# Kernel tuning notes

Hardware: AMD Instinct MI355X
Metric: run time of the kernel (lower is better)

Reference implementation:

```python
import jax, jax.numpy as jnp
import numpy as np

B, S, H = 2, 2048, 1024
NH = 16
HD = H // NH  # 64


def setup_inputs() -> dict:
    key = jax.random.key(0)
    ks = jax.random.split(key, 12)
    s = 1.0 / np.sqrt(H)
    return {
        "x_q": jax.random.normal(ks[0], (B, S, H), jnp.float32),
        "x_k": jax.random.normal(ks[1], (B, S, H), jnp.float32),
        "x_v": jax.random.normal(ks[2], (B, S, H), jnp.float32),
        "attention_mask": jax.random.randint(ks[3], (B, S), 0, 2, jnp.int32),
        "Wq": jax.random.normal(ks[4], (H, H), jnp.float32) * s,
        "bq": jnp.zeros((H,), jnp.float32),
        "Wk": jax.random.normal(ks[5], (H, H), jnp.float32) * s,
        "bk": jnp.zeros((H,), jnp.float32),
        "Wv": jax.random.normal(ks[6], (H, H), jnp.float32) * s,
        "bv": jnp.zeros((H,), jnp.float32),
        "Wo": jax.random.normal(ks[7], (H, H), jnp.float32) * s,
        "bo": jnp.zeros((H,), jnp.float32),
    }


def reference(x_q, x_k, x_v, attention_mask, Wq, bq, Wk, bk, Wv, bv, Wo, bo):
    b, s, h = x_q.shape
    # projections
    q = x_q @ Wq + bq
    k = x_k @ Wk + bk
    v = x_v @ Wv + bv
    # [B, NH, S, HD]
    q = q.reshape(b, s, NH, HD).transpose(0, 2, 1, 3)
    k = k.reshape(b, s, NH, HD).transpose(0, 2, 1, 3)
    v = v.reshape(b, s, NH, HD).transpose(0, 2, 1, 3)
    scores = jnp.einsum("bhqd,bhkd->bhqk", q, k) / jnp.sqrt(jnp.float32(HD))
    # key-padding mask: 1 -> keep (0 bias), else -inf; broadcast [B,1,1,S]
    bias = jnp.where(attention_mask == 1, 0.0, -jnp.inf).astype(scores.dtype)
    scores = scores + bias[:, None, None, :]
    attn = jax.nn.softmax(scores, axis=-1)
    # dropout prob = 0.0 (eval / deterministic): identity
    out = jnp.einsum("bhqk,bhkd->bhqd", attn, v)
    out = out.transpose(0, 2, 1, 3).reshape(b, s, h)
    return out @ Wo + bo
```

## Files before the change

### kernel.cpp

```cpp
#include <hip/hip_runtime.h>

#define DEVI static __device__ __forceinline__

typedef unsigned short u16;
typedef unsigned int u32;
typedef __attribute__((ext_vector_type(8))) __bf16 bf16x8;
typedef __attribute__((ext_vector_type(8))) short short8;
typedef __attribute__((ext_vector_type(4))) float f32x4;
typedef __attribute__((ext_vector_type(16))) float f32x16;
typedef __attribute__((ext_vector_type(4))) u32 u32x4;

DEVI u16 f2bf(float f) {
  union { float f; u32 u; } v; v.f = f;
  u32 r = v.u + 0x7fffu + ((v.u >> 16) & 1u);
  return (u16)(r >> 16);
}

DEVI u16 bfc(float f) {
  union { __bf16 b; u16 u; } v; v.b = (__bf16)f; return v.u;
}

DEVI u32 pk2bf(float lo, float hi) {
  union { struct { __bf16 l, h; } s; u32 u; } c;
  c.s.l = (__bf16)lo; c.s.h = (__bf16)hi;
  return c.u;
}

DEVI void gload16(const void* g, void* l) {
  __builtin_amdgcn_global_load_lds(
      (const __attribute__((address_space(1))) void*)g,
      (__attribute__((address_space(3))) void*)l,
      16, 0, 0);
}

__global__ void k_prep(const float* __restrict__ W0, const float* __restrict__ W1,
                       const float* __restrict__ W2, const float* __restrict__ W3,
                       u16* __restrict__ Wtb,
                       const int* __restrict__ msk, float* __restrict__ bias,
                       const float* __restrict__ xq, const float* __restrict__ xk,
                       const float* __restrict__ xv, u16* __restrict__ xbf) {
  const int z = blockIdx.z;
  const int tid = threadIdx.y * 32 + threadIdx.x;
  if (z == 4) {
    if (blockIdx.x < 16 && blockIdx.y == 0) {
      const int i = blockIdx.x * 256 + tid;
      bias[i] = (msk[i] == 1) ? 0.f : -1e30f;
    }
    return;
  }
  if (z >= 5) {
    const int xi = z - 5;
    const float* in = (xi == 0) ? xq : ((xi == 1) ? xk : xv);
    u16* out = xbf + (size_t)xi * 4194304;
    const int lin = (blockIdx.y * 32 + blockIdx.x) * 256 + tid;
#pragma unroll
    for (int j = 0; j < 4; ++j) {
      const int idx = j * 262144 + lin;
      const float4 v = reinterpret_cast<const float4*>(in)[idx];
      ushort4 s;
      s.x = f2bf(v.x); s.y = f2bf(v.y); s.z = f2bf(v.z); s.w = f2bf(v.w);
      reinterpret_cast<ushort4*>(out)[idx] = s;
    }
    return;
  }
  const float* W = (z == 0) ? W0 : ((z == 1) ? W1 : ((z == 2) ? W2 : W3));
  u16* Wt = Wtb + (size_t)z * 1024 * 1024;
  __shared__ float tl[32][33];
  const int n0 = blockIdx.x * 32, k0 = blockIdx.y * 32;
  const int tx = threadIdx.x, ty = threadIdx.y;
#pragma unroll
  for (int r = ty; r < 32; r += 8)
    tl[r][tx] = W[(size_t)(k0 + r) * 1024 + n0 + tx];
  __syncthreads();
#pragma unroll
  for (int r = ty; r < 32; r += 8)
    Wt[(size_t)(n0 + r) * 1024 + k0 + tx] = f2bf(tl[tx][r]);
}

DEVI void store1(u16* C, size_t i, float v) { C[i] = f2bf(v); }
DEVI void store1(float* C, size_t i, float v) { C[i] = v; }

template <typename OutT, int BN>
__global__ __launch_bounds__(256, 2) void k_gemm_bt(
    const u16* __restrict__ Abase, long aZ,
    const u16* __restrict__ Btbase, long bZ,
    const float* __restrict__ bias0, const float* __restrict__ bias1,
    const float* __restrict__ bias2,
    float s0, float s1, float s2,
    OutT* __restrict__ Cbase, long cZ, u16* __restrict__ Vt,
    int M, int N, int K) {
  const int z = blockIdx.z;
  const u16* A  = Abase + (size_t)z * aZ;
  const u16* Bt = Btbase + (size_t)z * bZ;
  OutT* C = Cbase + (size_t)z * cZ;
  const float* bias = (z == 0) ? bias0 : ((z == 1) ? bias1 : bias2);
  const float scl = (z == 0) ? s0 : ((z == 1) ? s1 : s2);

  constexpr int NF = BN / 32;
  __shared__ u16 lsA[128 * 32];
  __shared__ u16 lsB[BN * 32];

  const int t = threadIdx.x;
  const int w = t >> 6, ln = t & 63;
  const int l15 = ln & 15, lhi = ln >> 4;
  const int wr = w >> 1, wc = w & 1;
  const int m0 = blockIdx.x * 128, n0 = blockIdx.y * BN;

  f32x4 acc[4][NF] = {};

  for (int kt = 0; kt < K; kt += 32) {
#pragma unroll
    for (int i = 0; i < 2; ++i) {
      const int li = i * 256 + t;
      const int row = li >> 2, cb = (li & 3) << 3;
      gload16(A + (size_t)(m0 + row) * K + kt + cb,
              (char*)lsA + (i * 256 + w * 64) * 16);
    }
#pragma unroll
    for (int i = 0; i < BN / 64; ++i) {
      const int li = i * 256 + t;
      const int row = li >> 2, cb = (li & 3) << 3;
      gload16(Bt + (size_t)(n0 + row) * K + kt + cb,
              (char*)lsB + (i * 256 + w * 64) * 16);
    }
    __syncthreads();

    bf16x8 af[4], bf_[NF];
#pragma unroll
    for (int m = 0; m < 4; ++m)
      af[m] = *reinterpret_cast<const bf16x8*>(
          &lsA[(wr * 64 + m * 16 + l15) * 32 + lhi * 8]);
#pragma unroll
    for (int n = 0; n < NF; ++n)
      bf_[n] = *reinterpret_cast<const bf16x8*>(
          &lsB[(wc * (BN / 2) + n * 16 + l15) * 32 + lhi * 8]);
#pragma unroll
    for (int m = 0; m < 4; ++m)
#pragma unroll
      for (int n = 0; n < NF; ++n)
        acc[m][n] = __builtin_amdgcn_mfma_f32_16x16x32_bf16(af[m], bf_[n], acc[m][n], 0, 0, 0);
    __syncthreads();
  }

  if (Vt != nullptr && z == 2) {
#pragma unroll
    for (int n = 0; n < NF; ++n) {
      const int c = n0 + wc * (BN / 2) + n * 16 + l15;
      const float bv = bias[c];
#pragma unroll
      for (int m = 0; m < 4; ++m) {
        const int r = m0 + wr * 64 + m * 16 + lhi * 4;
        ushort4 s4;
#pragma unroll
        for (int j = 0; j < 4; ++j) ((u16*)&s4)[j] = f2bf(acc[m][n][j] + bv);
        *reinterpret_cast<ushort4*>(
            &Vt[((size_t)((r >> 11) * 1024 + c)) * 2048 + (r & 2047)]) = s4;
      }
    }
    return;
  }

#pragma unroll
  for (int n = 0; n < NF; ++n) {
    const int c = n0 + wc * (BN / 2) + n * 16 + l15;
    const float bv = bias[c];
#pragma unroll
    for (int m = 0; m < 4; ++m)
#pragma unroll
      for (int j = 0; j < 4; ++j) {
        const int r = m0 + wr * 64 + m * 16 + lhi * 4 + j;
        store1(C, (size_t)r * N + c, (acc[m][n][j] + bv) * scl);
      }
  }
}

__global__ __launch_bounds__(256, 2) void k_attn(
    const u16* __restrict__ Q, const u16* __restrict__ K, const u16* __restrict__ Vt,
    const float* __restrict__ MB, u16* __restrict__ O) {
  __shared__ u16 lsK[3][64][72];
  __shared__ u16 lsV[2][64][72];

  const int t = threadIdx.x, w = t >> 6, ln = t & 63;
  const int l31 = ln & 31, h = ln >> 5, h8 = h * 8;
  const int fid = blockIdx.x;
  const int xcd = fid & 7, slot = fid >> 3;
  const int pair = xcd * 4 + (slot >> 4);
  const int qt = slot & 15;
  const int hh = pair & 15, b = pair >> 4;

  const size_t rowQ = (size_t)b * 2048 + qt * 128 + w * 32;
  const int hc = hh * 64;

  const int srow = t >> 3, scol = (t & 7) << 3;
  const u16* Kg = K + ((size_t)b * 2048 + srow) * 1024 + hc + scol;
  const int half = t & 1;
  const int g16 = ((t & 7) >> 1) << 4;
  const u16* VgA = Vt + ((size_t)(b * 1024 + hc) + srow) * 2048 + g16 + 4 * half;
  const float* MBb = MB + b * 2048;

  bf16x8 qb[4];
#pragma unroll
  for (int ks = 0; ks < 4; ++ks)
    qb[ks] = *reinterpret_cast<const bf16x8*>(
        &Q[(rowQ + l31) * 1024 + hc + ks * 16 + h8]);

  f32x16 o[2];
#pragma unroll
  for (int i = 0; i < 16; ++i) { o[0][i] = 0.f; o[1][i] = 0.f; }
  float mrow = -1e30f, lsum = 0.f;

#pragma unroll
  for (int p = 0; p < 3; ++p) {
    const short8 a = *reinterpret_cast<const short8*>(Kg + (size_t)(p * 64) * 1024);
    const short8 c = *reinterpret_cast<const short8*>(Kg + (size_t)(p * 64 + 32) * 1024);
    *reinterpret_cast<short8*>(&lsK[p][srow][scol]) = a;
    *reinterpret_cast<short8*>(&lsK[p][32 + srow][scol]) = c;
  }
#pragma unroll
  for (int p = 0; p < 2; ++p) {
    const ushort4 a = *reinterpret_cast<const ushort4*>(VgA + p * 64);
    const ushort4 b4 = *reinterpret_cast<const ushort4*>(VgA + p * 64 + 8);
    const ushort4 c = *reinterpret_cast<const ushort4*>(VgA + 32 * 2048 + p * 64);
    const ushort4 d = *reinterpret_cast<const ushort4*>(VgA + 32 * 2048 + p * 64 + 8);
    *reinterpret_cast<ushort4*>(&lsV[p][srow][scol]) = a;
    *reinterpret_cast<ushort4*>(&lsV[p][srow][scol + 4]) = b4;
    *reinterpret_cast<ushort4*>(&lsV[p][32 + srow][scol]) = c;
    *reinterpret_cast<ushort4*>(&lsV[p][32 + srow][scol + 4]) = d;
  }
  __syncthreads();

  f32x16 stA[2], stB[2];
#pragma unroll
  for (int f = 0; f < 2; ++f)
#pragma unroll
    for (int rg = 0; rg < 4; ++rg) {
      const f32x4 bv = *reinterpret_cast<const f32x4*>(&MBb[f * 32 + rg * 8 + h * 4]);
#pragma unroll
      for (int jj = 0; jj < 4; ++jj) stA[f][rg * 4 + jj] = bv[jj];
    }
#pragma unroll
  for (int ks = 0; ks < 4; ++ks) {
    const bf16x8 kb0 = *reinterpret_cast<const bf16x8*>(&lsK[0][l31][ks * 16 + h8]);
    const bf16x8 kb1 = *reinterpret_cast<const bf16x8*>(&lsK[0][32 + l31][ks * 16 + h8]);
    stA[0] = __builtin_amdgcn_mfma_f32_32x32x16_bf16(kb0, qb[ks], stA[0], 0, 0, 0);
    stA[1] = __builtin_amdgcn_mfma_f32_32x32x16_bf16(kb1, qb[ks], stA[1], 0, 0, 0);
  }

#define ATTN_BODY(T, CUR, NXT, SW)                                                  \
  {                                                                                 \
    const int tK = ((T) + 3) & 31, tV = ((T) + 2) & 31, tB = ((T) + 1) & 31;        \
    const short8 rk0 = *reinterpret_cast<const short8*>(Kg + (size_t)(tK * 64) * 1024); \
    const short8 rk1 = *reinterpret_cast<const short8*>(Kg + (size_t)(tK * 64 + 32) * 1024); \
    const ushort4 rv0a = *reinterpret_cast<const ushort4*>(VgA + tV * 64);          \
    const ushort4 rv0b = *reinterpret_cast<const ushort4*>(VgA + tV * 64 + 8);      \
    const ushort4 rv1a = *reinterpret_cast<const ushort4*>(VgA + 32 * 2048 + tV * 64); \
    const ushort4 rv1b = *reinterpret_cast<const ushort4*>(VgA + 32 * 2048 + tV * 64 + 8); \
    const int sK = ((SW) == 2) ? 0 : (SW) + 1;                                      \
    _Pragma("unroll")                                                               \
    for (int f = 0; f < 2; ++f)                                                     \
      _Pragma("unroll")                                                             \
      for (int rg = 0; rg < 4; ++rg) {                                              \
        const f32x4 bv = *reinterpret_cast<const f32x4*>(                           \
            &MBb[tB * 64 + f * 32 + rg * 8 + h * 4]);                               \
        _Pragma("unroll")                                                           \
        for (int jj = 0; jj < 4; ++jj) NXT[f][rg * 4 + jj] = bv[jj];                \
      }                                                                             \
    __builtin_amdgcn_s_setprio(1);                                                  \
    _Pragma("unroll")                                                               \
    for (int ks = 0; ks < 4; ++ks) {                                                \
      const bf16x8 kb0 = *reinterpret_cast<const bf16x8*>(&lsK[sK][l31][ks * 16 + h8]); \
      const bf16x8 kb1 = *reinterpret_cast<const bf16x8*>(&lsK[sK][32 + l31][ks * 16 + h8]); \
      NXT[0] = __builtin_amdgcn_mfma_f32_32x32x16_bf16(kb0, qb[ks], NXT[0], 0, 0, 0); \
      NXT[1] = __builtin_amdgcn_mfma_f32_32x32x16_bf16(kb1, qb[ks], NXT[1], 0, 0, 0); \
    }                                                                               \
    __builtin_amdgcn_s_setprio(0);                                                  \
    float m0 = CUR[0][0], m1 = CUR[0][1], m2 = CUR[0][2], m3 = CUR[0][3];           \
    _Pragma("unroll")                                                               \
    for (int i = 4; i < 16; i += 4) {                                               \
      m0 = fmaxf(m0, CUR[0][i + 0]); m1 = fmaxf(m1, CUR[0][i + 1]);                 \
      m2 = fmaxf(m2, CUR[0][i + 2]); m3 = fmaxf(m3, CUR[0][i + 3]);                 \
    }                                                                               \
    _Pragma("unroll")                                                               \
    for (int i = 0; i < 16; i += 4) {                                               \
      m0 = fmaxf(m0, CUR[1][i + 0]); m1 = fmaxf(m1, CUR[1][i + 1]);                 \
      m2 = fmaxf(m2, CUR[1][i + 2]); m3 = fmaxf(m3, CUR[1][i + 3]);                 \
    }                                                                               \
    float tm = fmaxf(fmaxf(m0, m1), fmaxf(m2, m3));                                 \
    tm = fmaxf(tm, __shfl_xor(tm, 32, 64));                                         \
    const bool trig = tm > mrow + 8.f;                                              \
    if (__any(trig)) {                                                              \
      const float al = trig ? __builtin_amdgcn_exp2f(mrow - tm) : 1.f;              \
      if (trig) mrow = tm;                                                          \
      lsum *= al;                                                                   \
      _Pragma("unroll")                                                             \
      for (int f = 0; f < 2; ++f)                                                   \
        _Pragma("unroll")                                                           \
        for (int i = 0; i < 16; ++i) o[f][i] *= al;                                 \
    }                                                                               \
    float r0 = 0.f, r1 = 0.f, r2 = 0.f, r3 = 0.f;                                   \
    _Pragma("unroll")                                                               \
    for (int f = 0; f < 2; ++f)                                                     \
      _Pragma("unroll")                                                             \
      for (int i = 0; i < 16; i += 4) {                                             \
        const float p0 = __builtin_amdgcn_exp2f(CUR[f][i + 0] - mrow);              \
        const float p1 = __builtin_amdgcn_exp2f(CUR[f][i + 1] - mrow);              \
        const float p2 = __builtin_amdgcn_exp2f(CUR[f][i + 2] - mrow);              \
        const float p3 = __builtin_amdgcn_exp2f(CUR[f][i + 3] - mrow);              \
        CUR[f][i + 0] = p0; CUR[f][i + 1] = p1;                                     \
        CUR[f][i + 2] = p2; CUR[f][i + 3] = p3;                                     \
        r0 += p0; r1 += p1; r2 += p2; r3 += p3;                                     \
      }                                                                             \
    lsum += (r0 + r1) + (r2 + r3);                                                  \
    __builtin_amdgcn_s_setprio(1);                                                  \
    _Pragma("unroll")                                                               \
    for (int f = 0; f < 2; ++f) {                                                   \
      u32 pk[8];                                                                    \
      _Pragma("unroll")                                                             \
      for (int i = 0; i < 8; ++i)                                                   \
        pk[i] = pk2bf(CUR[f][2 * i], CUR[f][2 * i + 1]);                            \
      _Pragma("unroll")                                                             \
      for (int s = 0; s < 2; ++s) {                                                 \
        u32x4 pw;                                                                   \
        pw[0] = pk[4 * s + 0]; pw[1] = pk[4 * s + 1];                               \
        pw[2] = pk[4 * s + 2]; pw[3] = pk[4 * s + 3];                               \
        const bf16x8 pb = __builtin_bit_cast(bf16x8, pw);                           \
        const int ks = f * 2 + s;                                                   \
        _Pragma("unroll")                                                           \
        for (int df2 = 0; df2 < 2; ++df2) {                                         \
          const bf16x8 vt = *reinterpret_cast<const bf16x8*>(                       \
              &lsV[(T) & 1][df2 * 32 + l31][ks * 16 + h8]);                         \
          o[df2] = __builtin_amdgcn_mfma_f32_32x32x16_bf16(vt, pb, o[df2], 0, 0, 0); \
        }                                                                           \
      }                                                                             \
    }                                                                               \
    __builtin_amdgcn_s_setprio(0);                                                  \
    __syncthreads();                                                                \
    *reinterpret_cast<short8*>(&lsK[SW][srow][scol]) = rk0;                         \
    *reinterpret_cast<short8*>(&lsK[SW][32 + srow][scol]) = rk1;                    \
    *reinterpret_cast<ushort4*>(&lsV[(T) & 1][srow][scol]) = rv0a;                  \
    *reinterpret_cast<ushort4*>(&lsV[(T) & 1][srow][scol + 4]) = rv0b;              \
    *reinterpret_cast<ushort4*>(&lsV[(T) & 1][32 + srow][scol]) = rv1a;             \
    *reinterpret_cast<ushort4*>(&lsV[(T) & 1][32 + srow][scol + 4]) = rv1b;         \
  }

  int sw = 0;
  for (int t2 = 0; t2 < 32; t2 += 2) {
    ATTN_BODY(t2, stA, stB, sw);
    sw = (sw == 2) ? 0 : sw + 1;
    ATTN_BODY(t2 + 1, stB, stA, sw);
    sw = (sw == 2) ? 0 : sw + 1;
  }
#undef ATTN_BODY

  const float ltot = lsum + __shfl_xor(lsum, 32, 64);
  const float inv = 1.f / ltot;
#pragma unroll
  for (int df2 = 0; df2 < 2; ++df2)
#pragma unroll
    for (int rg = 0; rg < 4; ++rg) {
      ushort4 s4;
      s4.x = bfc(o[df2][rg * 4 + 0] * inv);
      s4.y = bfc(o[df2][rg * 4 + 1] * inv);
      s4.z = bfc(o[df2][rg * 4 + 2] * inv);
      s4.w = bfc(o[df2][rg * 4 + 3] * inv);
      *reinterpret_cast<ushort4*>(
          &O[(rowQ + l31) * 1024 + hc + df2 * 32 + rg * 8 + h * 4]) = s4;
    }
}

extern "C" void kernel_launch(void* const* d_in, const int* in_sizes, int n_in,
                              void* d_out, int out_size, void* d_ws, size_t ws_size,
                              hipStream_t stream) {
  const float* x_q = (const float*)d_in[0];
  const float* x_k = (const float*)d_in[1];
  const float* x_v = (const float*)d_in[2];
  const int*   msk = (const int*)d_in[3];
  const float* Wq  = (const float*)d_in[4];
  const float* bq  = (const float*)d_in[5];
  const float* Wk  = (const float*)d_in[6];
  const float* bk  = (const float*)d_in[7];
  const float* Wv  = (const float*)d_in[8];
  const float* bv  = (const float*)d_in[9];
  const float* Wo  = (const float*)d_in[10];
  const float* bo  = (const float*)d_in[11];

  const size_t NTOK = 4096, H = 1024;
  u16* xbf  = (u16*)d_ws;
  u16* wt   = xbf + 3 * NTOK * H;
  u16* qkv  = wt  + 4 * H * H;
  u16* aout = qkv + 3 * NTOK * H;
  float* mb = (float*)(aout + NTOK * H);
  u16* vtb  = qkv + 2 * NTOK * H;

  k_prep<<<dim3(32, 32, 8), dim3(32, 8), 0, stream>>>(
      Wq, Wk, Wv, Wo, wt, msk, mb, x_q, x_k, x_v, xbf);

  const float qscale = 0.125f * 1.4426950408889634f;
  k_gemm_bt<u16, 128><<<dim3(32, 8, 3), dim3(256), 0, stream>>>(
      xbf, (long)(NTOK * H), wt, (long)(H * H), bq, bk, bv,
      qscale, 1.f, 1.f,
      qkv, (long)(NTOK * H), vtb, 4096, 1024, 1024);

  k_attn<<<dim3(512), dim3(256), 0, stream>>>(
      qkv, qkv + NTOK * H, vtb, mb, aout);

  k_gemm_bt<float, 64><<<dim3(32, 16, 1), dim3(256), 0, stream>>>(
      aout, 0L, wt + 3 * H * H, 0L, bo, bo, bo,
      1.f, 1.f, 1.f,
      (float*)d_out, 0L, nullptr, 4096, 1024, 1024);
}
```

Baseline: 133.3 us.

## Split attention KV range in two and merge partials in a combine kernel

The attention kernel now splits each (batch, head, q-tile) over two halves of the key sequence, which doubles the grid to 1024 blocks. Each block writes a bf16 partial output plus its running max and sum. A new k_comb kernel merges the two halves with log-sum-exp weights. The K LDS ring shrinks from triple to double buffering and launch bounds rise to 4 blocks per CU to raise occupancy. The cost is an extra kernel launch, extra global traffic for the partials, and a second bf16 rounding of the output.

New measurement: 228.8 us. 1.72x slower.

```diff
diff --git a/kernel.cpp b/kernel.cpp
--- a/kernel.cpp
+++ b/kernel.cpp
@@ -18,6 +18,10 @@
 
 DEVI u16 bfc(float f) {
   union { __bf16 b; u16 u; } v; v.b = (__bf16)f; return v.u;
+}
+
+DEVI float bf2f(u16 u) {
+  union { u32 u; float f; } v; v.u = ((u32)u) << 16; return v.f;
 }
 
 DEVI u32 pk2bf(float lo, float hi) {
@@ -174,29 +178,30 @@
   }
 }
 
-__global__ __launch_bounds__(256, 2) void k_attn(
+__global__ __launch_bounds__(256, 4) void k_attn(
     const u16* __restrict__ Q, const u16* __restrict__ K, const u16* __restrict__ Vt,
-    const float* __restrict__ MB, u16* __restrict__ O) {
-  __shared__ u16 lsK[3][64][72];
+    const float* __restrict__ MB, u16* __restrict__ OP, float2* __restrict__ ml) {
+  __shared__ u16 lsK[2][64][72];
   __shared__ u16 lsV[2][64][72];
 
   const int t = threadIdx.x, w = t >> 6, ln = t & 63;
   const int l31 = ln & 31, h = ln >> 5, h8 = h * 8;
   const int fid = blockIdx.x;
   const int xcd = fid & 7, slot = fid >> 3;
-  const int pair = xcd * 4 + (slot >> 4);
-  const int qt = slot & 15;
+  const int pair = xcd * 4 + (slot >> 5);
+  const int rem = slot & 31;
+  const int s = rem & 1, qt = rem >> 1;
   const int hh = pair & 15, b = pair >> 4;
 
   const size_t rowQ = (size_t)b * 2048 + qt * 128 + w * 32;
   const int hc = hh * 64;
 
   const int srow = t >> 3, scol = (t & 7) << 3;
-  const u16* Kg = K + ((size_t)b * 2048 + srow) * 1024 + hc + scol;
+  const u16* Kg = K + ((size_t)b * 2048 + s * 1024 + srow) * 1024 + hc + scol;
   const int half = t & 1;
   const int g16 = ((t & 7) >> 1) << 4;
-  const u16* VgA = Vt + ((size_t)(b * 1024 + hc) + srow) * 2048 + g16 + 4 * half;
-  const float* MBb = MB + b * 2048;
+  const u16* VgA = Vt + ((size_t)(b * 1024 + hc) + srow) * 2048 + s * 1024 + g16 + 4 * half;
+  const float* MBb = MB + b * 2048 + s * 1024;
 
   bf16x8 qb[4];
 #pragma unroll
@@ -210,22 +215,19 @@
   float mrow = -1e30f, lsum = 0.f;
 
 #pragma unroll
-  for (int p = 0; p < 3; ++p) {
+  for (int p = 0; p < 2; ++p) {
     const short8 a = *reinterpret_cast<const short8*>(Kg + (size_t)(p * 64) * 1024);
     const short8 c = *reinterpret_cast<const short8*>(Kg + (size_t)(p * 64 + 32) * 1024);
     *reinterpret_cast<short8*>(&lsK[p][srow][scol]) = a;
     *reinterpret_cast<short8*>(&lsK[p][32 + srow][scol]) = c;
-  }
-#pragma unroll
-  for (int p = 0; p < 2; ++p) {
-    const ushort4 a = *reinterpret_cast<const ushort4*>(VgA + p * 64);
-    const ushort4 b4 = *reinterpret_cast<const ushort4*>(VgA + p * 64 + 8);
-    const ushort4 c = *reinterpret_cast<const ushort4*>(VgA + 32 * 2048 + p * 64);
-    const ushort4 d = *reinterpret_cast<const ushort4*>(VgA + 32 * 2048 + p * 64 + 8);
-    *reinterpret_cast<ushort4*>(&lsV[p][srow][scol]) = a;
-    *reinterpret_cast<ushort4*>(&lsV[p][srow][scol + 4]) = b4;
-    *reinterpret_cast<ushort4*>(&lsV[p][32 + srow][scol]) = c;
-    *reinterpret_cast<ushort4*>(&lsV[p][32 + srow][scol + 4]) = d;
+    const ushort4 va = *reinterpret_cast<const ushort4*>(VgA + p * 64);
+    const ushort4 vb = *reinterpret_cast<const ushort4*>(VgA + p * 64 + 8);
+    const ushort4 vc = *reinterpret_cast<const ushort4*>(VgA + 32 * 2048 + p * 64);
+    const ushort4 vd = *reinterpret_cast<const ushort4*>(VgA + 32 * 2048 + p * 64 + 8);
+    *reinterpret_cast<ushort4*>(&lsV[p][srow][scol]) = va;
+    *reinterpret_cast<ushort4*>(&lsV[p][srow][scol + 4]) = vb;
+    *reinterpret_cast<ushort4*>(&lsV[p][32 + srow][scol]) = vc;
+    *reinterpret_cast<ushort4*>(&lsV[p][32 + srow][scol + 4]) = vd;
   }
   __syncthreads();
 
@@ -246,16 +248,15 @@
     stA[1] = __builtin_amdgcn_mfma_f32_32x32x16_bf16(kb1, qb[ks], stA[1], 0, 0, 0);
   }
 
-#define ATTN_BODY(T, CUR, NXT, SW)                                                  \
+#define ATTN_BODY(T, CUR, NXT)                                                      \
   {                                                                                 \
-    const int tK = ((T) + 3) & 31, tV = ((T) + 2) & 31, tB = ((T) + 1) & 31;        \
-    const short8 rk0 = *reinterpret_cast<const short8*>(Kg + (size_t)(tK * 64) * 1024); \
-    const short8 rk1 = *reinterpret_cast<const short8*>(Kg + (size_t)(tK * 64 + 32) * 1024); \
-    const ushort4 rv0a = *reinterpret_cast<const ushort4*>(VgA + tV * 64);          \
-    const ushort4 rv0b = *reinterpret_cast<const ushort4*>(VgA + tV * 64 + 8);      \
-    const ushort4 rv1a = *reinterpret_cast<const ushort4*>(VgA + 32 * 2048 + tV * 64); \
-    const ushort4 rv1b = *reinterpret_cast<const ushort4*>(VgA + 32 * 2048 + tV * 64 + 8); \
-    const int sK = ((SW) == 2) ? 0 : (SW) + 1;                                      \
+    const int tN = ((T) + 2) & 15, tB = ((T) + 1) & 15;                             \
+    const short8 rk0 = *reinterpret_cast<const short8*>(Kg + (size_t)(tN * 64) * 1024); \
+    const short8 rk1 = *reinterpret_cast<const short8*>(Kg + (size_t)(tN * 64 + 32) * 1024); \
+    const ushort4 rv0a = *reinterpret_cast<const ushort4*>(VgA + tN * 64);          \
+    const ushort4 rv0b = *reinterpret_cast<const ushort4*>(VgA + tN * 64 + 8);      \
+    const ushort4 rv1a = *reinterpret_cast<const ushort4*>(VgA + 32 * 2048 + tN * 64); \
+    const ushort4 rv1b = *reinterpret_cast<const ushort4*>(VgA + 32 * 2048 + tN * 64 + 8); \
     _Pragma("unroll")                                                               \
     for (int f = 0; f < 2; ++f)                                                     \
       _Pragma("unroll")                                                             \
@@ -268,8 +269,10 @@
     __builtin_amdgcn_s_setprio(1);                                                  \
     _Pragma("unroll")                                                               \
     for (int ks = 0; ks < 4; ++ks) {                                                \
-      const bf16x8 kb0 = *reinterpret_cast<const bf16x8*>(&lsK[sK][l31][ks * 16 + h8]); \
-      const bf16x8 kb1 = *reinterpret_cast<const bf16x8*>(&lsK[sK][32 + l31][ks * 16 + h8]); \
+      const bf16x8 kb0 = *reinterpret_cast<const bf16x8*>(                          \
+          &lsK[((T) + 1) & 1][l31][ks * 16 + h8]);                                  \
+      const bf16x8 kb1 = *reinterpret_cast<const bf16x8*>(                          \
+          &lsK[((T) + 1) & 1][32 + l31][ks * 16 + h8]);                             \
       NXT[0] = __builtin_amdgcn_mfma_f32_32x32x16_bf16(kb0, qb[ks], NXT[0], 0, 0, 0); \
       NXT[1] = __builtin_amdgcn_mfma_f32_32x32x16_bf16(kb1, qb[ks], NXT[1], 0, 0, 0); \
     }                                                                               \
@@ -319,12 +322,12 @@
       for (int i = 0; i < 8; ++i)                                                   \
         pk[i] = pk2bf(CUR[f][2 * i], CUR[f][2 * i + 1]);                            \
       _Pragma("unroll")                                                             \
-      for (int s = 0; s < 2; ++s) {                                                 \
+      for (int ss = 0; ss < 2; ++ss) {                                              \
         u32x4 pw;                                                                   \
-        pw[0] = pk[4 * s + 0]; pw[1] = pk[4 * s + 1];                               \
-        pw[2] = pk[4 * s + 2]; pw[3] = pk[4 * s + 3];                               \
+        pw[0] = pk[4 * ss + 0]; pw[1] = pk[4 * ss + 1];                             \
+        pw[2] = pk[4 * ss + 2]; pw[3] = pk[4 * ss + 3];                             \
         const bf16x8 pb = __builtin_bit_cast(bf16x8, pw);                           \
-        const int ks = f * 2 + s;                                                   \
+        const int ks = f * 2 + ss;                                                  \
         _Pragma("unroll")                                                           \
         for (int df2 = 0; df2 < 2; ++df2) {                                         \
           const bf16x8 vt = *reinterpret_cast<const bf16x8*>(                       \
@@ -334,26 +337,27 @@
       }                                                                             \
     }                                                                               \
     __builtin_amdgcn_s_setprio(0);                                                  \
+        \
+    *reinterpret_cast<short8*>(&lsK[(T) & 1][srow][scol]) = rk0;                    \
+    *reinterpret_cast<short8*>(&lsK[(T) & 1][32 + srow][scol]) = rk1;               \
     __syncthreads();                                                                \
-    *reinterpret_cast<short8*>(&lsK[SW][srow][scol]) = rk0;                         \
-    *reinterpret_cast<short8*>(&lsK[SW][32 + srow][scol]) = rk1;                    \
+                   \
     *reinterpret_cast<ushort4*>(&lsV[(T) & 1][srow][scol]) = rv0a;                  \
     *reinterpret_cast<ushort4*>(&lsV[(T) & 1][srow][scol + 4]) = rv0b;              \
     *reinterpret_cast<ushort4*>(&lsV[(T) & 1][32 + srow][scol]) = rv1a;             \
     *reinterpret_cast<ushort4*>(&lsV[(T) & 1][32 + srow][scol + 4]) = rv1b;         \
   }
 
-  int sw = 0;
-  for (int t2 = 0; t2 < 32; t2 += 2) {
-    ATTN_BODY(t2, stA, stB, sw);
-    sw = (sw == 2) ? 0 : sw + 1;
-    ATTN_BODY(t2 + 1, stB, stA, sw);
-    sw = (sw == 2) ? 0 : sw + 1;
+  for (int t2 = 0; t2 < 16; t2 += 2) {
+    ATTN_BODY(t2, stA, stB);
+    ATTN_BODY(t2 + 1, stB, stA);
   }
 #undef ATTN_BODY
 
   const float ltot = lsum + __shfl_xor(lsum, 32, 64);
-  const float inv = 1.f / ltot;
+  const float inv = 1.f / fmaxf(ltot, 1e-37f);
+  const int qrow = qt * 128 + w * 32 + l31;
+  u16* OPr = OP + ((size_t)(s * 32 + pair) * 2048 + qrow) * 64;
 #pragma unroll
   for (int df2 = 0; df2 < 2; ++df2)
 #pragma unroll
@@ -363,9 +367,40 @@
       s4.y = bfc(o[df2][rg * 4 + 1] * inv);
       s4.z = bfc(o[df2][rg * 4 + 2] * inv);
       s4.w = bfc(o[df2][rg * 4 + 3] * inv);
-      *reinterpret_cast<ushort4*>(
-          &O[(rowQ + l31) * 1024 + hc + df2 * 32 + rg * 8 + h * 4]) = s4;
-    }
+      *reinterpret_cast<ushort4*>(&OPr[df2 * 32 + rg * 8 + h * 4]) = s4;
+    }
+  if (h == 0) {
+    float2 v; v.x = mrow; v.y = ltot;
+    ml[(size_t)(s * 32 + pair) * 2048 + qrow] = v;
+  }
+}
+
+__global__ __launch_bounds__(256) void k_comb(
+    const u16* __restrict__ OP, const float2* __restrict__ ml,
+    u16* __restrict__ aout) {
+  const int item = blockIdx.x * 256 + threadIdx.x;
+  const int dq = item & 15;
+  const int qrow = (item >> 4) & 2047;
+  const int pair = item >> 15;
+  const int hh = pair & 15, b = pair >> 4;
+  const float2 ml0 = ml[(size_t)pair * 2048 + qrow];
+  const float2 ml1 = ml[(size_t)(32 + pair) * 2048 + qrow];
+  const float ms = fmaxf(ml0.x, ml1.x);
+  float w0 = ml0.y * __builtin_amdgcn_exp2f(ml0.x - ms);
+  float w1 = ml1.y * __builtin_amdgcn_exp2f(ml1.x - ms);
+  const float inv = 1.f / fmaxf(w0 + w1, 1e-37f);
+  w0 *= inv; w1 *= inv;
+  const ushort4 a = *reinterpret_cast<const ushort4*>(
+      &OP[((size_t)pair * 2048 + qrow) * 64 + dq * 4]);
+  const ushort4 c = *reinterpret_cast<const ushort4*>(
+      &OP[((size_t)(32 + pair) * 2048 + qrow) * 64 + dq * 4]);
+  ushort4 r;
+  r.x = bfc(w0 * bf2f(a.x) + w1 * bf2f(c.x));
+  r.y = bfc(w0 * bf2f(a.y) + w1 * bf2f(c.y));
+  r.z = bfc(w0 * bf2f(a.z) + w1 * bf2f(c.z));
+  r.w = bfc(w0 * bf2f(a.w) + w1 * bf2f(c.w));
+  *reinterpret_cast<ushort4*>(
+      &aout[((size_t)b * 2048 + qrow) * 1024 + hh * 64 + dq * 4]) = r;
 }
 
 extern "C" void kernel_launch(void* const* d_in, const int* in_sizes, int n_in,
@@ -390,7 +425,9 @@
   u16* qkv  = wt  + 4 * H * H;
   u16* aout = qkv + 3 * NTOK * H;
   float* mb = (float*)(aout + NTOK * H);
+  float2* ml = (float2*)(mb + 4096);
   u16* vtb  = qkv + 2 * NTOK * H;
+  u16* op   = xbf;
 
   k_prep<<<dim3(32, 32, 8), dim3(32, 8), 0, stream>>>(
       Wq, Wk, Wv, Wo, wt, msk, mb, x_q, x_k, x_v, xbf);
@@ -401,8 +438,10 @@
       qscale, 1.f, 1.f,
       qkv, (long)(NTOK * H), vtb, 4096, 1024, 1024);
 
-  k_attn<<<dim3(512), dim3(256), 0, stream>>>(
-      qkv, qkv + NTOK * H, vtb, mb, aout);
+  k_attn<<<dim3(1024), dim3(256), 0, stream>>>(
+      qkv, qkv + NTOK * H, vtb, mb, op, ml);
+
+  k_comb<<<dim3(4096), dim3(256), 0, stream>>>(op, ml, aout);
 
   k_gemm_bt<float, 64><<<dim3(32, 16, 1), dim3(256), 0, stream>>>(
       aout, 0L, wt + 3 * H * H, 0L, bo, bo, bo,
```
